# Kernel tuning notes

Hardware: AMD Instinct MI355X
Metric: run time of the kernel (lower is better)

The kernel has to match this reference:

```python
import jax, jax.numpy as jnp
import numpy as np

NUM_FEATURES = 2344
ACC = 8
B = 262144
N_ACTIVE = 38


def setup_inputs() -> dict:
    key = jax.random.key(0)
    k1, k2, k3, k4, k5, k6, k7 = jax.random.split(key, 7)
    return {
        "black_features": jax.random.randint(k1, (B, N_ACTIVE), 0, NUM_FEATURES, dtype=jnp.int64 if jax.config.jax_enable_x64 else jnp.int32).astype(jnp.int32),
        "white_features": jax.random.randint(k2, (B, N_ACTIVE), 0, NUM_FEATURES, dtype=jnp.int64 if jax.config.jax_enable_x64 else jnp.int32).astype(jnp.int32),
        "stm": jax.random.randint(k3, (B,), 0, 2, dtype=jnp.int32),
        "l1_weight": jax.random.normal(k4, (NUM_FEATURES, ACC), dtype=jnp.float32) * 0.1,
        "l1_bias": jax.random.normal(k5, (ACC,), dtype=jnp.float32) * 0.1,
        "l2_weight": jax.random.normal(k6, (1, 2 * ACC), dtype=jnp.float32) * 0.1,
        "l2_bias": jax.random.normal(k7, (1,), dtype=jnp.float32) * 0.1,
    }


def reference(black_features, white_features, stm, l1_weight, l1_bias, l2_weight, l2_bias):
    # sparse embedding sum accumulators: [B, N_ACTIVE, ACC] -> [B, ACC]
    b_acc = jnp.take(l1_weight, black_features, axis=0).sum(axis=1) + l1_bias
    w_acc = jnp.take(l1_weight, white_features, axis=0).sum(axis=1) + l1_bias
    # side-to-move ordered concat: [B, 2*ACC]
    bw = jnp.concatenate([b_acc, w_acc], axis=1)
    wb = jnp.concatenate([w_acc, b_acc], axis=1)
    acc = jnp.where((stm == 0)[:, None], bw, wb)
    acc = jnp.clip(acc, 0.0, 1.0)
    # tiny linear: [B, 16] @ [16, 1] + [1]
    return acc @ l2_weight.T + l2_bias
```

## Files before the change

kernel.cpp:

```cpp
#include <hip/hip_runtime.h>
#include <stdint.h>

#define NF   2344
#define ACCW 8
#define NA   38
#define TPB  512

__device__ __forceinline__ unsigned short f32_to_bf16(float f) {
    unsigned u = __float_as_uint(f);
    u += 0x7FFFu + ((u >> 16) & 1u);
    return (unsigned short)(u >> 16);
}
__device__ __forceinline__ float bf16_lo(unsigned u) { return __uint_as_float(u << 16); }
__device__ __forceinline__ float bf16_hi(unsigned u) { return __uint_as_float(u & 0xFFFF0000u); }

__global__ __launch_bounds__(TPB, 4) void nnue_fwd(
    const int* __restrict__ bfeat, const int* __restrict__ wfeat,
    const int* __restrict__ stm,
    const float* __restrict__ w1, const float* __restrict__ b1,
    const float* __restrict__ w2, const float* __restrict__ b2,
    float* __restrict__ out, int nbatch)
{
    __shared__ unsigned short tbl[NF * ACCW];

    for (int j = threadIdx.x; j < (NF * ACCW) / 4; j += TPB) {
        float4 v = reinterpret_cast<const float4*>(w1)[j];
        unsigned lo = (unsigned)f32_to_bf16(v.x) | ((unsigned)f32_to_bf16(v.y) << 16);
        unsigned hi = (unsigned)f32_to_bf16(v.z) | ((unsigned)f32_to_bf16(v.w) << 16);
        reinterpret_cast<uint2*>(tbl)[j] = make_uint2(lo, hi);
    }
    __syncthreads();

    const int t = blockIdx.x * TPB + threadIdx.x;
    const int e = t >> 1;
    const int h = t & 1;
    if (e >= nbatch) return;

    const int* __restrict__ bp = bfeat + (long)e * NA;
    const int* __restrict__ wp = wfeat + (long)e * NA;

#define G(acc, idx) { \
        uint4 r = *reinterpret_cast<const uint4*>( \
            reinterpret_cast<const char*>(tbl) + ((unsigned)(idx) << 4)); \
        acc[0] += bf16_lo(r.x); acc[1] += bf16_hi(r.x); \
        acc[2] += bf16_lo(r.y); acc[3] += bf16_hi(r.y); \
        acc[4] += bf16_lo(r.z); acc[5] += bf16_hi(r.z); \
        acc[6] += bf16_lo(r.w); acc[7] += bf16_hi(r.w); }

    float accB[8] = {0,0,0,0,0,0,0,0};
    float accW[8] = {0,0,0,0,0,0,0,0};

    {
        int2 q[9];
#pragma unroll
        for (int j = 0; j < 9; ++j)
            q[j] = *reinterpret_cast<const int2*>(bp + 4 * j + 2 * h);
        const int2 qt = *reinterpret_cast<const int2*>(bp + 36);
#pragma unroll
        for (int j = 0; j < 9; ++j) { G(accB, q[j].x); G(accB, q[j].y); }
        G(accB, h ? qt.y : qt.x);
    }

    asm volatile("" ::: "memory");

    {
        int2 q[9];
#pragma unroll
        for (int j = 0; j < 9; ++j)
            q[j] = *reinterpret_cast<const int2*>(wp + 4 * j + 2 * h);
        const int2 qt = *reinterpret_cast<const int2*>(wp + 36);
#pragma unroll
        for (int j = 0; j < 9; ++j) { G(accW, q[j].x); G(accW, q[j].y); }
        G(accW, h ? qt.y : qt.x);
    }
#undef G

    float mine[8];
#pragma unroll
    for (int k = 0; k < 8; ++k) {
        float fb = accB[k] + __shfl_xor(accB[k], 1);
        float fw = accW[k] + __shfl_xor(accW[k], 1);
        mine[k] = (h ? fw : fb) + b1[k];
    }

    float dlo = 0.f, dhi = 0.f;
#pragma unroll
    for (int k = 0; k < 8; ++k) {
        float v = fminf(fmaxf(mine[k], 0.f), 1.f);
        dlo += v * w2[k];
        dhi += v * w2[8 + k];
    }

    const int s = stm[e];
    const float m = (((s == 0)) == (h == 0)) ? dlo : dhi;
    const float o = __shfl_xor(m, 1);
    if (h == 0) out[e] = m + o + b2[0];
}

extern "C" void kernel_launch(void* const* d_in, const int* in_sizes, int n_in,
                              void* d_out, int out_size, void* d_ws, size_t ws_size,
                              hipStream_t stream) {
    const int*   bfeat = (const int*)  d_in[0];
    const int*   wfeat = (const int*)  d_in[1];
    const int*   stm   = (const int*)  d_in[2];
    const float* w1    = (const float*)d_in[3];
    const float* b1    = (const float*)d_in[4];
    const float* w2    = (const float*)d_in[5];
    const float* b2    = (const float*)d_in[6];
    float* out = (float*)d_out;

    const int nbatch  = in_sizes[2];
    const long nthread = (long)nbatch * 2;
    const int grid = (int)((nthread + TPB - 1) / TPB);
    nnue_fwd<<<grid, TPB, 0, stream>>>(bfeat, wfeat, stm, w1, b1, w2, b2, out, nbatch);
}
```

Baseline: 21.95 us.

## Process one batch element per thread instead of splitting across thread pairs

Each thread now handles a whole batch element. It reads its 38 black and 38 white feature indices with 16-byte vector loads and accumulates both colours itself, so the cross-lane shuffles and the half-split logic go away. The grid is halved, which also halves how many times each block converts the weight table to bf16 and stages it in LDS. In exchange, each thread does twice the serial LDS gathers, there are fewer waves to hide latency, and the 16-byte index loads are only 8-byte aligned for odd elements.

After: 36.43 us. 1.66x slower.

```diff
diff --git a/kernel.cpp b/kernel.cpp
--- a/kernel.cpp
+++ b/kernel.cpp
@@ -31,13 +31,8 @@
     }
     __syncthreads();
 
-    const int t = blockIdx.x * TPB + threadIdx.x;
-    const int e = t >> 1;
-    const int h = t & 1;
+    const int e = blockIdx.x * TPB + threadIdx.x;
     if (e >= nbatch) return;
-
-    const int* __restrict__ bp = bfeat + (long)e * NA;
-    const int* __restrict__ wp = wfeat + (long)e * NA;
 
 #define G(acc, idx) { \
         uint4 r = *reinterpret_cast<const uint4*>( \
@@ -47,54 +42,37 @@
         acc[4] += bf16_lo(r.z); acc[5] += bf16_hi(r.z); \
         acc[6] += bf16_lo(r.w); acc[7] += bf16_hi(r.w); }
 
+#define GATHER_COLOR(acc, basep) { \
+        const char* cb = reinterpret_cast<const char*>(basep); \
+        int4 q[10]; \
+        _Pragma("unroll") \
+        for (int j = 0; j < 9; ++j) \
+            q[j] = *reinterpret_cast<const int4*>(cb + 16 * j); \
+        q[9] = *reinterpret_cast<const int4*>(cb + 136); \
+        _Pragma("unroll") \
+        for (int j = 0; j < 9; ++j) { \
+            G(acc, q[j].x); G(acc, q[j].y); G(acc, q[j].z); G(acc, q[j].w); \
+        } \
+        G(acc, q[9].z); G(acc, q[9].w); }
+
     float accB[8] = {0,0,0,0,0,0,0,0};
     float accW[8] = {0,0,0,0,0,0,0,0};
 
-    {
-        int2 q[9];
-#pragma unroll
-        for (int j = 0; j < 9; ++j)
-            q[j] = *reinterpret_cast<const int2*>(bp + 4 * j + 2 * h);
-        const int2 qt = *reinterpret_cast<const int2*>(bp + 36);
-#pragma unroll
-        for (int j = 0; j < 9; ++j) { G(accB, q[j].x); G(accB, q[j].y); }
-        G(accB, h ? qt.y : qt.x);
-    }
-
-    asm volatile("" ::: "memory");
-
-    {
-        int2 q[9];
-#pragma unroll
-        for (int j = 0; j < 9; ++j)
-            q[j] = *reinterpret_cast<const int2*>(wp + 4 * j + 2 * h);
-        const int2 qt = *reinterpret_cast<const int2*>(wp + 36);
-#pragma unroll
-        for (int j = 0; j < 9; ++j) { G(accW, q[j].x); G(accW, q[j].y); }
-        G(accW, h ? qt.y : qt.x);
-    }
+    GATHER_COLOR(accB, bfeat + (long)e * NA);
+    GATHER_COLOR(accW, wfeat + (long)e * NA);
+#undef GATHER_COLOR
 #undef G
 
-    float mine[8];
+    float dbl = 0.f, dbh = 0.f, dwl = 0.f, dwh = 0.f;
 #pragma unroll
     for (int k = 0; k < 8; ++k) {
-        float fb = accB[k] + __shfl_xor(accB[k], 1);
-        float fw = accW[k] + __shfl_xor(accW[k], 1);
-        mine[k] = (h ? fw : fb) + b1[k];
+        float bv = fminf(fmaxf(accB[k] + b1[k], 0.f), 1.f);
+        float wv = fminf(fmaxf(accW[k] + b1[k], 0.f), 1.f);
+        dbl += bv * w2[k]; dbh += bv * w2[8 + k];
+        dwl += wv * w2[k]; dwh += wv * w2[8 + k];
     }
-
-    float dlo = 0.f, dhi = 0.f;
-#pragma unroll
-    for (int k = 0; k < 8; ++k) {
-        float v = fminf(fmaxf(mine[k], 0.f), 1.f);
-        dlo += v * w2[k];
-        dhi += v * w2[8 + k];
-    }
-
     const int s = stm[e];
-    const float m = (((s == 0)) == (h == 0)) ? dlo : dhi;
-    const float o = __shfl_xor(m, 1);
-    if (h == 0) out[e] = m + o + b2[0];
+    out[e] = b2[0] + (s == 0 ? (dbl + dwh) : (dbh + dwl));
 }
 
 extern "C" void kernel_launch(void* const* d_in, const int* in_sizes, int n_in,
@@ -109,8 +87,7 @@
     const float* b2    = (const float*)d_in[6];
     float* out = (float*)d_out;
 
-    const int nbatch  = in_sizes[2];
-    const long nthread = (long)nbatch * 2;
-    const int grid = (int)((nthread + TPB - 1) / TPB);
+    const int nbatch = in_sizes[2];
+    const int grid = (nbatch + TPB - 1) / TPB;
     nnue_fwd<<<grid, TPB, 0, stream>>>(bfeat, wfeat, stm, w1, b1, w2, b2, out, nbatch);
 }
```
